# Optimization experiments

Measured on AMD Instinct MI355X. Metric: run time of the kernel, lower is better.

## Reference

```python
import jax, jax.numpy as jnp
import numpy as np

SEQ_LEN = 4096
N_FEAT = 2048
N_PADD = 128


def setup_inputs() -> dict:
    key = jax.random.key(0)
    kx, kw = jax.random.split(key)
    x = jax.random.normal(kx, (SEQ_LEN, N_FEAT), dtype=jnp.float32)
    # Fused QKV dense: features = 3 * n_feat
    W = jax.random.normal(kw, (N_FEAT, 3 * N_FEAT), dtype=jnp.float32) * (1.0 / np.sqrt(N_FEAT))
    b = jnp.zeros((3 * N_FEAT,), dtype=jnp.float32)
    return {"x": x, "W": W, "b": b, "n_padd": N_PADD}


def reference(x, W, b, n_padd):
    # Fused QKV projection, split along feature axis (as in nn.Dense + jnp.split)
    qkv = x @ W + b  # [S, 3F]
    q, k, v = jnp.split(qkv, 3, axis=1)  # each [S, F]
    S, F = q.shape
    idx = jnp.arange(S)
    # scores[i, j] = q_i . k_j / sqrt(F)
    scores = (q @ k.T) * (1.0 / jnp.sqrt(jnp.float32(F)))  # [S, S]
    seq_mask = idx >= n_padd                      # valid (non-padding) positions
    causal = idx[None, :] <= idx[:, None]         # j <= i
    mask = causal & seq_mask[None, :]             # kernel: causal_mask & seq_mask
    row_valid = seq_mask                          # rows < n_padd are not computed/stored
    neg_inf = jnp.float32(-jnp.inf)
    scores = jnp.where(mask, scores, neg_inf)
    # Fully-masked (padding) rows would softmax to NaN; neutralize then zero output.
    scores = jnp.where(row_valid[:, None], scores, 0.0)
    att = jax.nn.softmax(scores, axis=-1)         # row-wise stable softmax
    out = att @ v                                 # [S, F]
    out = jnp.where(row_valid[:, None], out, 0.0)  # padded rows produce zeros
    return out
```

## Files before the change

kernel.cpp:

```cpp
#include <hip/hip_runtime.h>
#include <cstdint>
#include <cstddef>

typedef unsigned short u16;
typedef short v8s __attribute__((ext_vector_type(8)));
typedef float v4f __attribute__((ext_vector_type(4)));

constexpr int SEQ = 4096;
constexpr int FEAT = 2048;
constexpr int F3 = 6144;


__device__ __forceinline__ u16 f2bf(float f) {
  union { float f; uint32_t u; } v; v.f = f;
  uint32_t r = v.u + 0x7FFFu + ((v.u >> 16) & 1u);
  return (u16)(r >> 16);
}

__device__ __forceinline__ float bf2f(u16 s) {
  union { uint32_t u; float f; } v; v.u = ((uint32_t)s) << 16;
  return v.f;
}

__device__ __forceinline__ void gld_lds16(const u16* g, u16* l) {
  __builtin_amdgcn_global_load_lds(
      (const __attribute__((address_space(1))) void*)g,
      (__attribute__((address_space(3))) void*)l, 16, 0, 0);
}


__global__ void cvt_f32_bf16(const float* __restrict__ in, u16* __restrict__ out, int n8) {
  int i = blockIdx.x * 256 + threadIdx.x;
  if (i >= n8) return;
  const float4* p = (const float4*)in + (size_t)i * 2;
  float4 a = p[0], b = p[1];
  union { u16 s[8]; uint4 v; } u;
  u.s[0] = f2bf(a.x); u.s[1] = f2bf(a.y); u.s[2] = f2bf(a.z); u.s[3] = f2bf(a.w);
  u.s[4] = f2bf(b.x); u.s[5] = f2bf(b.y); u.s[6] = f2bf(b.z); u.s[7] = f2bf(b.w);
  *(uint4*)(out + (size_t)i * 8) = u.v;
}

__global__ void transp_f2b(const float* __restrict__ in, int ldin,
                           u16* __restrict__ out, int ldout) {
  __shared__ float tile[32][33];
  int c0 = blockIdx.x * 32, r0 = blockIdx.y * 32;
  int tx = threadIdx.x, ty = threadIdx.y;
#pragma unroll
  for (int p = 0; p < 4; ++p)
    tile[ty + 8 * p][tx] = in[(size_t)(r0 + ty + 8 * p) * ldin + c0 + tx];
  __syncthreads();
#pragma unroll
  for (int p = 0; p < 4; ++p)
    out[(size_t)(c0 + ty + 8 * p) * ldout + r0 + tx] = f2bf(tile[tx][ty + 8 * p]);
}

__global__ void transp_b2b(const u16* __restrict__ in, int ldin,
                           u16* __restrict__ out, int ldout) {
  __shared__ u16 tile[32][33];
  int c0 = blockIdx.x * 32, r0 = blockIdx.y * 32;
  int tx = threadIdx.x, ty = threadIdx.y;
#pragma unroll
  for (int p = 0; p < 4; ++p)
    tile[ty + 8 * p][tx] = in[(size_t)(r0 + ty + 8 * p) * ldin + c0 + tx];
  __syncthreads();
#pragma unroll
  for (int p = 0; p < 4; ++p)
    out[(size_t)(c0 + ty + 8 * p) * ldout + r0 + tx] = tile[tx][ty + 8 * p];
}


#define BAR()  asm volatile("s_barrier" ::: "memory")
#define VMC3() asm volatile("s_waitcnt vmcnt(3)" ::: "memory")

template<int LDA, int LDB, int LDC, int OUTMODE ,
         int ADDB, int CAUSAL, int SWZ>
__global__ __launch_bounds__(512, 4) void gemmw(
    const u16* __restrict__ A, const u16* __restrict__ B,
    void* __restrict__ Cv, int K,
    const float* __restrict__ bias, float scale) {
  int bi, bj;
  if (SWZ) {
    const int gx = gridDim.x;
    const int nwg = gx * gridDim.y;
    const int b = blockIdx.y * gx + blockIdx.x;
    const int cpx = nwg >> 3;
    const int s = (b & 7) * cpx + (b >> 3);
    bj = s % gx;  bi = s / gx;
  } else { bj = blockIdx.x; bi = blockIdx.y; }
  int ks, ke;
  if (CAUSAL) {
    if (blockIdx.z) bi = (int)gridDim.y - 1 - bi;
    const int kq = (bi + 1) * 64;
    ks = blockIdx.z ? kq : 0;  ke = ks + kq;
  } else { ks = 0; ke = K; }
  const int i0 = bi * 128, j0 = bj * 256;

  __shared__ u16 As[3][4096];
  __shared__ u16 Bs[3][8192];

  const int t = threadIdx.x;
  const int w = t >> 6, l = t & 63;
  const int wr = w >> 2, wc = w & 3;
  const int lm = l & 15, lq = l >> 4;
  const int lqs = ((lq + (lm >> 1)) & 3) * 8;

  const int srow = t >> 2;
  const int scol = (((t & 3) - ((t >> 3) & 3)) & 3) * 8;
  const u16* Ag = A + (size_t)(i0 + srow) * LDA + scol;
  const u16* Bg = B + (size_t)(j0 + srow) * LDB + scol;
  u16* Al = &As[0][0] + w * 512;
  u16* Bl = &Bs[0][0] + w * 512;

  v4f acc[4][4];
#pragma unroll
  for (int a = 0; a < 4; ++a)
#pragma unroll
    for (int b2 = 0; b2 < 4; ++b2)
      acc[a][b2] = v4f{0.f, 0.f, 0.f, 0.f};

  gld_lds16(Ag + ks, Al);
  gld_lds16(Bg + ks, Bl);
  gld_lds16(Bg + 128 * LDB + ks, Bl + 4096);
  gld_lds16(Ag + ks + 32, Al + 4096);
  gld_lds16(Bg + ks + 32, Bl + 8192);
  gld_lds16(Bg + 128 * LDB + ks + 32, Bl + 8192 + 4096);
  VMC3(); BAR();

  const int nt = (ke - ks) >> 5;
  int bufr = 0;
  int k2 = ks + 64;
  for (int tt = 0; tt < nt; ++tt) {
    v8s af[4], bf4[4];
    const u16* Ar = &As[0][0] + bufr * 4096 + (wr * 64 + lm) * 32 + lqs;
    const u16* Br = &Bs[0][0] + bufr * 8192 + (wc * 64 + lm) * 32 + lqs;
#pragma unroll
    for (int mi = 0; mi < 4; ++mi) af[mi] = *(const v8s*)(Ar + mi * 512);
#pragma unroll
    for (int ni = 0; ni < 4; ++ni) bf4[ni] = *(const v8s*)(Br + ni * 512);
    const int sb = (bufr + 2 >= 3) ? bufr - 1 : bufr + 2;
    const int kst = (k2 < ke) ? k2 : ks;
    gld_lds16(Ag + kst, Al + sb * 4096);
    gld_lds16(Bg + kst, Bl + sb * 8192);
    gld_lds16(Bg + 128 * LDB + kst, Bl + sb * 8192 + 4096);
    __builtin_amdgcn_s_setprio(1);
#pragma unroll
    for (int mi = 0; mi < 4; ++mi)
#pragma unroll
      for (int ni = 0; ni < 4; ++ni)
        acc[mi][ni] = __builtin_amdgcn_mfma_f32_16x16x32_bf16(af[mi], bf4[ni], acc[mi][ni], 0, 0, 0);
    __builtin_amdgcn_s_setprio(0);
    VMC3(); BAR();
    bufr = (bufr == 2) ? 0 : bufr + 1;
    k2 += 32;
  }

#pragma unroll
  for (int mi = 0; mi < 4; ++mi) {
#pragma unroll
    for (int ni = 0; ni < 4; ++ni) {
      const int cc = j0 + wc * 64 + ni * 16 + lm;
      const float badd = ADDB ? bias[cc] : 0.f;
#pragma unroll
      for (int r = 0; r < 4; ++r) {
        const int rr = i0 + wr * 64 + mi * 16 + lq * 4 + r;
        if (OUTMODE == 0)
          ((u16*)Cv)[(size_t)rr * LDC + cc] = f2bf(acc[mi][ni][r] * scale + badd);
        else
          atomicAdd((float*)Cv + (size_t)rr * LDC + cc, acc[mi][ni][r]);
      }
    }
  }
}

__global__ __launch_bounds__(256) void softmax_rows(
    const u16* __restrict__ S0,
    u16* __restrict__ att, const int* __restrict__ npad_p) {
  const int i = blockIdx.x;
  const int np = *npad_p;
  const int kend = ((i >> 7) + 1) << 7;
  const u16* r0 = S0 + (size_t)i * SEQ;
  u16* arow = att + (size_t)i * SEQ;
  const int t = threadIdx.x;

  float m = -3.0e38f, s = 0.f;
  for (int j = np + t; j <= i; j += 256) {
    float v = bf2f(r0[j]);
    if (v > m) { s = s * __expf(m - v) + 1.f; m = v; }
    else       { s += __expf(v - m); }
  }
#pragma unroll
  for (int off = 32; off > 0; off >>= 1) {
    float mo = __shfl_xor(m, off);
    float so = __shfl_xor(s, off);
    float M = fmaxf(m, mo);
    s = s * __expf(m - M) + so * __expf(mo - M);
    m = M;
  }
  __shared__ float sm[4], ss[4];
  const int w = t >> 6, l = t & 63;
  if (l == 0) { sm[w] = m; ss[w] = s; }
  __syncthreads();
  const float M = fmaxf(fmaxf(sm[0], sm[1]), fmaxf(sm[2], sm[3]));
  const float Ssum = ss[0] * __expf(sm[0] - M) + ss[1] * __expf(sm[1] - M) +
                     ss[2] * __expf(sm[2] - M) + ss[3] * __expf(sm[3] - M);
  const float inv = 1.f / Ssum;

  for (int j0b = t * 8; j0b < kend; j0b += 2048) {
    union { u16 s8[8]; uint4 v; } u;
#pragma unroll
    for (int q = 0; q < 8; ++q) {
      const int j = j0b + q;
      float a = 0.f;
      if (j >= np && j <= i)
        a = __expf(bf2f(r0[j]) - M) * inv;
      u.s8[q] = f2bf(a);
    }
    *(uint4*)(arow + j0b) = u.v;
  }
}


extern "C" void kernel_launch(void* const* d_in, const int* in_sizes, int n_in,
                              void* d_out, int out_size, void* d_ws, size_t ws_size,
                              hipStream_t stream) {
  const float* x = (const float*)d_in[0];
  const float* W = (const float*)d_in[1];
  const float* b = (const float*)d_in[2];
  const int* npad = (const int*)d_in[3];
  float* out = (float*)d_out;

  char* p = (char*)d_ws;
  u16* xb = (u16*)p;
  u16* Wt = (u16*)(p + (size_t)SEQ * FEAT * 2);
  u16* att = (u16*)p;
  p += (size_t)SEQ * FEAT * 2 + (size_t)F3 * FEAT * 2;
  u16* qkvb = (u16*)p;  p += (size_t)SEQ * F3 * 2;
  u16* vt   = (u16*)p;  p += (size_t)FEAT * SEQ * 2;
  u16* sc0  = (u16*)p;  p += (size_t)SEQ * SEQ * 2;
  if (ws_size < (size_t)(p - (char*)d_ws)) return;

  const float scale = 0.02209708691207961f;

  hipMemsetAsync(d_out, 0, (size_t)SEQ * FEAT * sizeof(float), stream);

  cvt_f32_bf16<<<SEQ * FEAT / 8 / 256, 256, 0, stream>>>(x, xb, SEQ * FEAT / 8);
  transp_f2b<<<dim3(F3 / 32, FEAT / 32), dim3(32, 8), 0, stream>>>(W, F3, Wt, FEAT);
  gemmw<FEAT, FEAT, F3, 0, 1, 0, 1><<<dim3(F3 / 256, SEQ / 128), 512, 0, stream>>>(
      xb, Wt, (void*)qkvb, FEAT, b, 1.0f);
  transp_b2b<<<dim3(FEAT / 32, SEQ / 32), dim3(32, 8), 0, stream>>>(
      qkvb + 2 * FEAT, F3, vt, SEQ);
  gemmw<F3, F3, SEQ, 0, 0, 0, 1><<<dim3(SEQ / 256, SEQ / 128), 512, 0, stream>>>(
      qkvb, qkvb + FEAT, (void*)sc0, FEAT, nullptr, scale);
  softmax_rows<<<SEQ, 256, 0, stream>>>(sc0, att, npad);
  gemmw<SEQ, SEQ, FEAT, 1, 0, 1, 0><<<dim3(FEAT / 256, SEQ / 128, 2), 512, 0, stream>>>(
      att, vt, (void*)out, 0, nullptr, 1.0f);
}
```

Baseline: 410.1 us.

## Shrink GEMM tiles to 128x128 and compute only causal lower-triangle score tiles

Shrinks the GEMM workgroup from 512 threads with 128x256 tiles to 256 threads with 128x128 tiles. The QK^T score GEMM now launches a 1D grid covering only the lower-triangular tile pairs, with tile coordinates recovered by a triangular index inverse. This skips the upper-triangle score tiles that causal masking discards. It also software-pipelines the B-fragment LDS loads one iteration ahead and changes the swizzle order. The cost is more workgroups and less reuse per tile in the other GEMMs.

```diff
diff --git a/kernel.cpp b/kernel.cpp
--- a/kernel.cpp
+++ b/kernel.cpp
@@ -1,6 +1,7 @@
 #include <hip/hip_runtime.h>
 #include <cstdint>
 #include <cstddef>
+#include <cmath>
 
 typedef unsigned short u16;
 typedef short v8s __attribute__((ext_vector_type(8)));
@@ -69,47 +70,72 @@
 }
 
 
-#define BAR()  asm volatile("s_barrier" ::: "memory")
-#define VMC3() asm volatile("s_waitcnt vmcnt(3)" ::: "memory")
-
-template<int LDA, int LDB, int LDC, int OUTMODE ,
+#define BARW()  asm volatile("s_barrier" ::: "memory")
+#define VMC4() asm volatile("s_waitcnt vmcnt(4)" ::: "memory")
+
+#define STAGE(SB, KO) do { \
+  gld_lds16(Ag + (KO), &As[SB][0] + w * 512); \
+  gld_lds16(Ag + (size_t)64 * LDA_ + (KO), &As[SB][0] + w * 512 + 2048); \
+  gld_lds16(Bg + (KO), &Bs[SB][0] + w * 512); \
+  gld_lds16(Bg + (size_t)64 * LDB_ + (KO), &Bs[SB][0] + w * 512 + 2048); \
+} while (0)
+
+#define LOADA(BUF) do { _Pragma("unroll") \
+  for (int mi = 0; mi < 4; ++mi) \
+    af[mi] = *(const v8s*)(&As[BUF][0] + (wr * 64 + mi * 16 + lm) * 32 + lqs); \
+} while (0)
+
+#define LOADB(BUF) do { _Pragma("unroll") \
+  for (int ni = 0; ni < 4; ++ni) \
+    bf4[ni] = *(const v8s*)(&Bs[BUF][0] + (wc * 64 + ni * 16 + lm) * 32 + lqs); \
+} while (0)
+
+template<int LDA_, int LDB_, int LDC_, int OUTMODE ,
          int ADDB, int CAUSAL, int SWZ>
-__global__ __launch_bounds__(512, 4) void gemmw(
+__global__ __launch_bounds__(256, 3) void gemmw(
     const u16* __restrict__ A, const u16* __restrict__ B,
     void* __restrict__ Cv, int K,
     const float* __restrict__ bias, float scale) {
-  int bi, bj;
-  if (SWZ) {
-    const int gx = gridDim.x;
-    const int nwg = gx * gridDim.y;
-    const int b = blockIdx.y * gx + blockIdx.x;
-    const int cpx = nwg >> 3;
+  int bi, bj, ks, ke;
+  if (CAUSAL == 2) {
+    const int b = blockIdx.x;
+    const int cpx = gridDim.x >> 3;
     const int s = (b & 7) * cpx + (b >> 3);
-    bj = s % gx;  bi = s / gx;
-  } else { bj = blockIdx.x; bi = blockIdx.y; }
-  int ks, ke;
-  if (CAUSAL) {
+    bi = (int)((sqrtf(8.f * s + 1.f) - 1.f) * 0.5f);
+    while ((bi + 1) * (bi + 2) / 2 <= s) ++bi;
+    while (bi * (bi + 1) / 2 > s) --bi;
+    bj = s - bi * (bi + 1) / 2;
+    ks = 0; ke = K;
+  } else if (CAUSAL == 1) {
+    bi = blockIdx.y; bj = blockIdx.x;
     if (blockIdx.z) bi = (int)gridDim.y - 1 - bi;
     const int kq = (bi + 1) * 64;
     ks = blockIdx.z ? kq : 0;  ke = ks + kq;
-  } else { ks = 0; ke = K; }
-  const int i0 = bi * 128, j0 = bj * 256;
+  } else {
+    if (SWZ) {
+      const int gx = gridDim.x, gy = gridDim.y;
+      const int b = blockIdx.y * gx + blockIdx.x;
+      const int cpx = (gx * gy) >> 3;
+      const int s = (b & 7) * cpx + (b >> 3);
+      bi = s % gy;  bj = s / gy;
+    } else { bj = blockIdx.x; bi = blockIdx.y; }
+    ks = 0; ke = K;
+  }
+  const int i0 = bi * 128, j0 = bj * 128;
 
   __shared__ u16 As[3][4096];
-  __shared__ u16 Bs[3][8192];
+  __shared__ u16 Bs[3][4096];
 
   const int t = threadIdx.x;
   const int w = t >> 6, l = t & 63;
-  const int wr = w >> 2, wc = w & 3;
+  const int wr = w >> 1, wc = w & 1;
   const int lm = l & 15, lq = l >> 4;
   const int lqs = ((lq + (lm >> 1)) & 3) * 8;
 
   const int srow = t >> 2;
   const int scol = (((t & 3) - ((t >> 3) & 3)) & 3) * 8;
-  const u16* Ag = A + (size_t)(i0 + srow) * LDA + scol;
-  const u16* Bg = B + (size_t)(j0 + srow) * LDB + scol;
-  u16* Al = &As[0][0] + w * 512;
-  u16* Bl = &Bs[0][0] + w * 512;
+  const u16* Ag = A + (size_t)(i0 + srow) * LDA_ + scol;
+  const u16* Bg = B + (size_t)(j0 + srow) * LDB_ + scol;
 
   v4f acc[4][4];
 #pragma unroll
@@ -118,30 +144,20 @@
     for (int b2 = 0; b2 < 4; ++b2)
       acc[a][b2] = v4f{0.f, 0.f, 0.f, 0.f};
 
-  gld_lds16(Ag + ks, Al);
-  gld_lds16(Bg + ks, Bl);
-  gld_lds16(Bg + 128 * LDB + ks, Bl + 4096);
-  gld_lds16(Ag + ks + 32, Al + 4096);
-  gld_lds16(Bg + ks + 32, Bl + 8192);
-  gld_lds16(Bg + 128 * LDB + ks + 32, Bl + 8192 + 4096);
-  VMC3(); BAR();
+  v8s af[4], bf4[4];
+
+  STAGE(0, ks); STAGE(1, ks + 32);
+  VMC4(); BARW();
+  LOADB(0);
 
   const int nt = (ke - ks) >> 5;
   int bufr = 0;
   int k2 = ks + 64;
   for (int tt = 0; tt < nt; ++tt) {
-    v8s af[4], bf4[4];
-    const u16* Ar = &As[0][0] + bufr * 4096 + (wr * 64 + lm) * 32 + lqs;
-    const u16* Br = &Bs[0][0] + bufr * 8192 + (wc * 64 + lm) * 32 + lqs;
-#pragma unroll
-    for (int mi = 0; mi < 4; ++mi) af[mi] = *(const v8s*)(Ar + mi * 512);
-#pragma unroll
-    for (int ni = 0; ni < 4; ++ni) bf4[ni] = *(const v8s*)(Br + ni * 512);
     const int sb = (bufr + 2 >= 3) ? bufr - 1 : bufr + 2;
     const int kst = (k2 < ke) ? k2 : ks;
-    gld_lds16(Ag + kst, Al + sb * 4096);
-    gld_lds16(Bg + kst, Bl + sb * 8192);
-    gld_lds16(Bg + 128 * LDB + kst, Bl + sb * 8192 + 4096);
+    STAGE(sb, kst);
+    LOADA(bufr);
     __builtin_amdgcn_s_setprio(1);
 #pragma unroll
     for (int mi = 0; mi < 4; ++mi)
@@ -149,8 +165,10 @@
       for (int ni = 0; ni < 4; ++ni)
         acc[mi][ni] = __builtin_amdgcn_mfma_f32_16x16x32_bf16(af[mi], bf4[ni], acc[mi][ni], 0, 0, 0);
     __builtin_amdgcn_s_setprio(0);
-    VMC3(); BAR();
-    bufr = (bufr == 2) ? 0 : bufr + 1;
+    VMC4(); BARW();
+    const int nb = (bufr == 2) ? 0 : bufr + 1;
+    LOADB(nb);
+    bufr = nb;
     k2 += 32;
   }
 
@@ -164,9 +182,9 @@
       for (int r = 0; r < 4; ++r) {
         const int rr = i0 + wr * 64 + mi * 16 + lq * 4 + r;
         if (OUTMODE == 0)
-          ((u16*)Cv)[(size_t)rr * LDC + cc] = f2bf(acc[mi][ni][r] * scale + badd);
+          ((u16*)Cv)[(size_t)rr * LDC_ + cc] = f2bf(acc[mi][ni][r] * scale + badd);
         else
-          atomicAdd((float*)Cv + (size_t)rr * LDC + cc, acc[mi][ni][r]);
+          atomicAdd((float*)Cv + (size_t)rr * LDC_ + cc, acc[mi][ni][r]);
       }
     }
   }
@@ -245,13 +263,13 @@
 
   cvt_f32_bf16<<<SEQ * FEAT / 8 / 256, 256, 0, stream>>>(x, xb, SEQ * FEAT / 8);
   transp_f2b<<<dim3(F3 / 32, FEAT / 32), dim3(32, 8), 0, stream>>>(W, F3, Wt, FEAT);
-  gemmw<FEAT, FEAT, F3, 0, 1, 0, 1><<<dim3(F3 / 256, SEQ / 128), 512, 0, stream>>>(
+  gemmw<FEAT, FEAT, F3, 0, 1, 0, 1><<<dim3(F3 / 128, SEQ / 128), 256, 0, stream>>>(
       xb, Wt, (void*)qkvb, FEAT, b, 1.0f);
   transp_b2b<<<dim3(FEAT / 32, SEQ / 32), dim3(32, 8), 0, stream>>>(
       qkvb + 2 * FEAT, F3, vt, SEQ);
-  gemmw<F3, F3, SEQ, 0, 0, 0, 1><<<dim3(SEQ / 256, SEQ / 128), 512, 0, stream>>>(
+  gemmw<F3, F3, SEQ, 0, 0, 2, 0><<<dim3(32 * 33 / 2), 256, 0, stream>>>(
       qkvb, qkvb + FEAT, (void*)sc0, FEAT, nullptr, scale);
   softmax_rows<<<SEQ, 256, 0, stream>>>(sc0, att, npad);
-  gemmw<SEQ, SEQ, FEAT, 1, 0, 1, 0><<<dim3(FEAT / 256, SEQ / 128, 2), 512, 0, stream>>>(
+  gemmw<SEQ, SEQ, FEAT, 1, 0, 1, 0><<<dim3(FEAT / 128, SEQ / 128, 2), 256, 0, stream>>>(
       att, vt, (void*)out, 0, nullptr, 1.0f);
 }
```

Measured after the change: 401.9 us. -2.0%, faster.
